# Optimization experiments

Measured on AMD Instinct MI355X. Metric: run time of the kernel, lower is better.

## Reference

```python
import jax, jax.numpy as jnp
import numpy as np

N_FFT = 4096
N_STAGES = 3
N_CHUNKS = 2 ** N_STAGES


def _mod_seq(order):
    mset = [0]
    for o in range(order):
        step = 2 ** o
        mset = [x + d for x in mset for d in (0, step)]
    return mset


def _perm_matrix(N, order):
    m = np.zeros((N, N), dtype=np.float32)
    base = 2 ** order
    k = 0
    for p in _mod_seq(order):
        for j in range(N // base):
            m[j * base + p, k] = 1.0
            k += 1
    return m


def setup_inputs() -> dict:
    key = jax.random.key(0)
    x = jax.random.normal(key, (8, 512, N_FFT), dtype=jnp.float32)
    perm = jnp.asarray(_perm_matrix(N_FFT, N_STAGES))
    return {"x": x, "perm": perm}


def reference(x, perm):
    # y[..., k] = sum_i x[..., i] * perm[i, k]  (dense matmul by one-hot permutation)
    y = jnp.matmul(x, perm)  # [B, T, N_FFT]
    return tuple(jnp.split(y, N_CHUNKS, axis=-1))  # N_CHUNKS arrays of [B, T, N_FFT // N_CHUNKS]
```

## Files before the change

kernel.cpp:

```cpp
#include <hip/hip_runtime.h>


#define COLS_TOTAL  (8u * 512u * 512u)
#define TILE_COLS   1024
#define BLOCK       256

__global__ __launch_bounds__(BLOCK) void
FFTPermuter_2748779070248_kernel(const float4* __restrict__ x4,
                                 float4* __restrict__ out4) {
    __shared__ __align__(16) float lds[8 * TILE_COLS];

    const int    tid   = threadIdx.x;
    const size_t tile  = blockIdx.x;
    const size_t base4 = tile * 2048;

#pragma unroll
    for (int k = 0; k < 8; ++k) {
        const int e4 = k * BLOCK + tid;
        float4 v = x4[base4 + e4];
        const int col = e4 >> 1;
        const int ph0 = (e4 & 1) * 4;
        lds[(ph0 + 0) * TILE_COLS + col] = v.x;
        lds[(ph0 + 1) * TILE_COLS + col] = v.y;
        lds[(ph0 + 2) * TILE_COLS + col] = v.z;
        lds[(ph0 + 3) * TILE_COLS + col] = v.w;
    }
    __syncthreads();

    const int ms[8] = {0, 4, 2, 6, 1, 5, 3, 7};
    const size_t colbase4 = tile * (TILE_COLS / 4);
#pragma unroll
    for (int c = 0; c < 8; ++c) {
        const int p = ms[c];
        const float4 o = *(const float4*)&lds[p * TILE_COLS + 4 * tid];
        out4[(size_t)c * (COLS_TOTAL / 4) + colbase4 + tid] = o;
    }
}

extern "C" void kernel_launch(void* const* d_in, const int* in_sizes, int n_in,
                              void* d_out, int out_size, void* d_ws, size_t ws_size,
                              hipStream_t stream) {
    const float4* x4   = (const float4*)d_in[0];
    float4*       out4 = (float4*)d_out;

    const int grid = COLS_TOTAL / TILE_COLS;
    FFTPermuter_2748779070248_kernel<<<grid, BLOCK, 0, stream>>>(x4, out4);
}
```

Baseline: 155.1 us.

## Replace LDS transpose with register shuffle, grid-stride loop and nontemporal accesses

Removes the shared-memory staging and barrier. Each thread now loads eight consecutive float4 (32 floats) and rebuilds the eight output float4 in registers. The launch becomes a fixed 512-block grid-stride loop, and loads and stores use nontemporal builtins to avoid polluting the cache. The cost is per-thread input loads that are strided by 128 bytes across lanes, so each wavefront load instruction is less coalesced. Register pressure also rises.

Result: slower. 166.4 us (+7.3%).

```diff
diff --git a/kernel.cpp b/kernel.cpp
--- a/kernel.cpp
+++ b/kernel.cpp
@@ -1,48 +1,48 @@
 #include <hip/hip_runtime.h>
 
 
+typedef float v4f __attribute__((ext_vector_type(4)));
+
 #define COLS_TOTAL  (8u * 512u * 512u)
-#define TILE_COLS   1024
+#define NGROUPS     (COLS_TOTAL / 4)
 #define BLOCK       256
+#define GRID        512
+#define ITERS       (NGROUPS / (GRID * BLOCK))
 
 __global__ __launch_bounds__(BLOCK) void
-FFTPermuter_2748779070248_kernel(const float4* __restrict__ x4,
-                                 float4* __restrict__ out4) {
-    __shared__ __align__(16) float lds[8 * TILE_COLS];
+FFTPermuter_2748779070248_kernel(const v4f* __restrict__ x4,
+                                 v4f* __restrict__ out4) {
+    const int stride = GRID * BLOCK;
+    int g = blockIdx.x * BLOCK + threadIdx.x;
 
-    const int    tid   = threadIdx.x;
-    const size_t tile  = blockIdx.x;
-    const size_t base4 = tile * 2048;
+    const int ms[8] = {0, 4, 2, 6, 1, 5, 3, 7};
 
 #pragma unroll
-    for (int k = 0; k < 8; ++k) {
-        const int e4 = k * BLOCK + tid;
-        float4 v = x4[base4 + e4];
-        const int col = e4 >> 1;
-        const int ph0 = (e4 & 1) * 4;
-        lds[(ph0 + 0) * TILE_COLS + col] = v.x;
-        lds[(ph0 + 1) * TILE_COLS + col] = v.y;
-        lds[(ph0 + 2) * TILE_COLS + col] = v.z;
-        lds[(ph0 + 3) * TILE_COLS + col] = v.w;
-    }
-    __syncthreads();
+    for (int it = 0; it < ITERS; ++it, g += stride) {
+        v4f v[8];
+#pragma unroll
+        for (int m = 0; m < 8; ++m)
+            v[m] = __builtin_nontemporal_load(&x4[(size_t)g * 8 + m]);
 
-    const int ms[8] = {0, 4, 2, 6, 1, 5, 3, 7};
-    const size_t colbase4 = tile * (TILE_COLS / 4);
 #pragma unroll
-    for (int c = 0; c < 8; ++c) {
-        const int p = ms[c];
-        const float4 o = *(const float4*)&lds[p * TILE_COLS + 4 * tid];
-        out4[(size_t)c * (COLS_TOTAL / 4) + colbase4 + tid] = o;
+        for (int c = 0; c < 8; ++c) {
+            const int p  = ms[c];
+            const int hi = p >> 2, lo = p & 3;
+            v4f o;
+            o.x = v[0 + hi][lo];
+            o.y = v[2 + hi][lo];
+            o.z = v[4 + hi][lo];
+            o.w = v[6 + hi][lo];
+            __builtin_nontemporal_store(o, &out4[(size_t)c * (COLS_TOTAL / 4) + g]);
+        }
     }
 }
 
 extern "C" void kernel_launch(void* const* d_in, const int* in_sizes, int n_in,
                               void* d_out, int out_size, void* d_ws, size_t ws_size,
                               hipStream_t stream) {
-    const float4* x4   = (const float4*)d_in[0];
-    float4*       out4 = (float4*)d_out;
+    const v4f* x4   = (const v4f*)d_in[0];
+    v4f*       out4 = (v4f*)d_out;
 
-    const int grid = COLS_TOTAL / TILE_COLS;
-    FFTPermuter_2748779070248_kernel<<<grid, BLOCK, 0, stream>>>(x4, out4);
+    FFTPermuter_2748779070248_kernel<<<GRID, BLOCK, 0, stream>>>(x4, out4);
 }
```
